# Kernel tuning notes

Measured on AMD Instinct MI355X. Metric: run time of the kernel, lower is better.

Reference implementation:

```python
import jax, jax.numpy as jnp
import numpy as np

N_EXPERTS = 8
TOP_K = 2
LB_COEF = 0.01
D_MODEL = 1024
D_FF = 4096


def setup_inputs() -> dict:
    key = jax.random.key(0)
    k_x, k_r, k_w1, k_w2, k_w3 = jax.random.split(key, 5)
    x = jax.random.normal(k_x, (2, 1024, D_MODEL), dtype=jnp.float32)
    # nn.Linear(d_model, n_experts, bias=False).weight has shape (E, d_model)
    router_w = jax.random.normal(k_r, (N_EXPERTS, D_MODEL), dtype=jnp.float32) * 0.02
    # stacked expert weights; stored pre-transposed for x @ W contractions
    w1 = jax.random.normal(k_w1, (N_EXPERTS, D_MODEL, D_FF), dtype=jnp.float32) * 0.02
    w3 = jax.random.normal(k_w3, (N_EXPERTS, D_MODEL, D_FF), dtype=jnp.float32) * 0.02
    w2 = jax.random.normal(k_w2, (N_EXPERTS, D_FF, D_MODEL), dtype=jnp.float32) * 0.02
    return {"x": x, "router_w": router_w, "w1": w1, "w3": w3, "w2": w2}


def reference(x, router_w, w1, w3, w2):
    B, T, C = x.shape
    xf = x.reshape(-1, C)                      # (N, C), N = B*T
    N = xf.shape[0]

    router_logits = xf @ router_w.T            # (N, E)
    top_v, top_i = jax.lax.top_k(router_logits, TOP_K)
    top_p = jax.nn.softmax(top_v, axis=-1)     # (N, K)

    # combine weight per (token, expert): sum of top-k probs routed to expert e
    comb = jnp.zeros((N, N_EXPERTS), dtype=xf.dtype)
    comb = comb.at[jnp.arange(N)[:, None], top_i].add(top_p)  # (N, E)

    # grouped SwiGLU FFN across all experts (dense-equivalent of masked loop;
    # tokens with zero combine weight contribute nothing)
    gate = jax.nn.silu(jnp.einsum("tc,ecf->etf", xf, w1))     # (E, N, F)
    up = jnp.einsum("tc,ecf->etf", xf, w3)                    # (E, N, F)
    expert_out = jnp.einsum("etf,efc->etc", gate * up, w2)    # (E, N, C)
    out = jnp.einsum("etc,te->tc", expert_out, comb)          # (N, C)

    router_probs = jax.nn.softmax(router_logits, axis=-1)
    expert_probs = router_probs.mean(axis=0)                  # (E,)
    aux_loss = LB_COEF * N_EXPERTS * jnp.sum(expert_probs * expert_probs)

    return out.reshape(B, T, C), aux_loss
```

## Files before the change

### kernel.cpp

```cpp
#include <hip/hip_runtime.h>
#include <hip/hip_bf16.h>
#include <hip/hip_fp16.h>

#define NTOK 2048
#define DM   1024
#define DF   4096
#define NE   8
#define NROWS (NTOK * 2)
#define NSPLIT 4
#define KSPL (DF / NSPLIT)
#define FFN1_NG (32 * 16 * 8)

typedef _Float16 f16x8 __attribute__((ext_vector_type(8)));
typedef float    f32x4 __attribute__((ext_vector_type(4)));
typedef unsigned u32x2 __attribute__((ext_vector_type(2)));

__device__ __forceinline__ void gload_lds16(const void* g, void* l) {
    __builtin_amdgcn_global_load_lds(
        (const __attribute__((address_space(1))) void*)g,
        (__attribute__((address_space(3))) void*)l, 16, 0, 0);
}

__device__ __forceinline__ u32x2 pack4(float4 v) {
    _Float16 a = (_Float16)v.x, b = (_Float16)v.y,
             c = (_Float16)v.z, d = (_Float16)v.w;
    unsigned ua = __builtin_bit_cast(unsigned short, a);
    unsigned ub = __builtin_bit_cast(unsigned short, b);
    unsigned uc = __builtin_bit_cast(unsigned short, c);
    unsigned ud = __builtin_bit_cast(unsigned short, d);
    u32x2 r;
    r[0] = ua | (ub << 16);
    r[1] = uc | (ud << 16);
    return r;
}

__global__ void k_init(int* counts, float* probs_sum) {
    int i = threadIdx.x;
    if (i < NE) { counts[i] = 0; probs_sum[i] = 0.f; }
}

__device__ __forceinline__ void transpose_tile(
    float* tile ,
    const float* __restrict__ src, _Float16* __restrict__ dst,
    int K, int N, int k0, int n0, int tid)
{
    int tk = tid >> 4, tn = (tid & 15) << 2;
#pragma unroll
    for (int r = 0; r < 4; r++) {
        float4 v = *(const float4*)(src + (size_t)(k0 + tk + (r << 4)) * N + n0 + tn);
        float* trow = &tile[(tk + (r << 4)) * 65 + tn];
        trow[0] = v.x; trow[1] = v.y; trow[2] = v.z; trow[3] = v.w;
    }
    __syncthreads();
    int on = tid >> 2, ok = (tid & 3) << 4;
    unsigned pk[8];
#pragma unroll
    for (int p2 = 0; p2 < 8; p2++) {
        _Float16 a = (_Float16)tile[(ok + 2 * p2) * 65 + on];
        _Float16 b = (_Float16)tile[(ok + 2 * p2 + 1) * 65 + on];
        pk[p2] = (unsigned)(*(unsigned short*)&a) | ((unsigned)(*(unsigned short*)&b) << 16);
    }
    _Float16* d = dst + (size_t)(n0 + on) * K + k0 + ok;
    *(uint4*)d       = make_uint4(pk[0], pk[1], pk[2], pk[3]);
    *(uint4*)(d + 8) = make_uint4(pk[4], pk[5], pk[6], pk[7]);
}

__global__ __launch_bounds__(256) void k_pre(
    const float* __restrict__ x, const float* __restrict__ rw,
    const float* __restrict__ w1, const float* __restrict__ w3,
    _Float16* __restrict__ WA, _Float16* __restrict__ WB,
    int* counts, float* probs_sum,
    int* pair_exp, int* pair_pos, float* topp)
{
    __shared__ float smem[64 * 65];
    int bid = blockIdx.x;
    int tid = threadIdx.x;

    if (bid >= 128) {
        int t = bid - 128;
        int z = t >> 10, xy = t & 1023;
        int e = z & 7;
        const float* src = ((z < 8) ? w1 : w3) + (size_t)e * DM * DF;
        _Float16* dst = ((z < 8) ? WA : WB) + (size_t)e * DF * DM;
        transpose_tile(smem, src, dst, DM, DF, (xy >> 6) << 6, (xy & 63) << 6, tid);
        return;
    }

    float* lprobs = smem;
    int* lcount = (int*)(smem + 8);
    int* lbase  = (int*)(smem + 16);
    if (tid < NE) { lprobs[tid] = 0.f; lcount[tid] = 0; }
    __syncthreads();

    int l16 = tid & 15;
    int t = bid * 16 + (tid >> 4);

    const float* xt = x + (size_t)t * DM;
    float acc[NE];
#pragma unroll
    for (int e = 0; e < NE; e++) acc[e] = 0.f;

#pragma unroll
    for (int i0 = 0; i0 < DM; i0 += 64) {
        int i = i0 + l16 * 4;
        float4 xv = *(const float4*)(xt + i);
#pragma unroll
        for (int e = 0; e < NE; e++) {
            float4 wv = *(const float4*)(rw + e * DM + i);
            acc[e] = fmaf(xv.x, wv.x, acc[e]);
            acc[e] = fmaf(xv.y, wv.y, acc[e]);
            acc[e] = fmaf(xv.z, wv.z, acc[e]);
            acc[e] = fmaf(xv.w, wv.w, acc[e]);
        }
    }
#pragma unroll
    for (int m = 1; m < 16; m <<= 1)
#pragma unroll
        for (int e = 0; e < NE; e++)
            acc[e] += __shfl_xor(acc[e], m);

    int i0e = 0, i1e = 0, r0 = 0, r1 = 0;
    if (l16 == 0) {
        float mx = acc[0];
#pragma unroll
        for (int e = 1; e < NE; e++) mx = fmaxf(mx, acc[e]);
        float p[NE]; float s = 0.f;
#pragma unroll
        for (int e = 0; e < NE; e++) { p[e] = expf(acc[e] - mx); s += p[e]; }
        float inv = 1.f / s;
#pragma unroll
        for (int e = 0; e < NE; e++) atomicAdd(&lprobs[e], p[e] * inv);

        i0e = 0;
#pragma unroll
        for (int e = 1; e < NE; e++) if (acc[e] > acc[i0e]) i0e = e;
        i1e = (i0e == 0) ? 1 : 0;
#pragma unroll
        for (int e = 0; e < NE; e++) if (e != i0e && acc[e] > acc[i1e]) i1e = e;

        float e1 = expf(acc[i1e] - acc[i0e]);
        float den = 1.f / (1.f + e1);
        topp[t * 2 + 0] = den;
        topp[t * 2 + 1] = e1 * den;
        pair_exp[t * 2 + 0] = i0e;
        pair_exp[t * 2 + 1] = i1e;
        r0 = atomicAdd(&lcount[i0e], 1);
        r1 = atomicAdd(&lcount[i1e], 1);
    }
    __syncthreads();
    if (tid < NE) {
        lbase[tid] = atomicAdd(&counts[tid], lcount[tid]);
        atomicAdd(&probs_sum[tid], lprobs[tid]);
    }
    __syncthreads();
    if (l16 == 0) {
        pair_pos[t * 2 + 0] = lbase[i0e] + r0;
        pair_pos[t * 2 + 1] = lbase[i1e] + r1;
    }
}

__global__ void k_offsets(const int* counts, const float* probs_sum,
                          int* eoff, float* out_aux)
{
    if (threadIdx.x == 0 && blockIdx.x == 0) {
        int off = 0;
        for (int e = 0; e < NE; e++) { eoff[e] = off; off += counts[e]; }
        eoff[NE] = off;
        float aux = 0.f;
        for (int e = 0; e < NE; e++) {
            float ep = probs_sum[e] / (float)NTOK;
            aux += ep * ep;
        }
        out_aux[0] = 0.01f * (float)NE * aux;
    }
}

__global__ __launch_bounds__(256) void k_gather(
    const float* __restrict__ x, const int* __restrict__ pair_exp,
    const int* __restrict__ pair_pos, const int* __restrict__ eoff,
    _Float16* __restrict__ Xg)
{
    int b = blockIdx.x;
    int t = b >> 1, s = b & 1;
    int e = pair_exp[t * 2 + s];
    int row = eoff[e] + pair_pos[t * 2 + s];
    int c = threadIdx.x << 2;
    float4 v = *(const float4*)(x + (size_t)t * DM + c);
    u32x2 o = pack4(v);
    *(u32x2*)(Xg + (size_t)row * DM + c) = o;
}

__global__ __launch_bounds__(256) void k_transpose(
    const float* __restrict__ W, _Float16* __restrict__ Wt, int K, int N)
{
    __shared__ float tile[64 * 65];
    int e = blockIdx.z;
    transpose_tile(tile, W + (size_t)e * K * N, Wt + (size_t)e * N * K,
                   K, N, blockIdx.y << 6, blockIdx.x << 6, threadIdx.x);
}

__global__ __launch_bounds__(256, 2) void k_ffn1(
    const _Float16* __restrict__ A, const _Float16* __restrict__ B1t,
    const _Float16* __restrict__ B3t, _Float16* __restrict__ H,
    const int* __restrict__ counts, const int* __restrict__ eoff,
    const float* __restrict__ w2, _Float16* __restrict__ W2T)
{
    __shared__ __align__(16) unsigned char smem[49152];
    int bid = blockIdx.x;
    int tid = threadIdx.x;

    if (bid >= FFN1_NG) {
        int t = bid - FFN1_NG;
        int e = t >> 10, xy = t & 1023;
        transpose_tile((float*)smem, w2 + (size_t)e * DF * DM,
                       W2T + (size_t)e * DM * DF,
                       DF, DM, (xy >> 4) << 6, (xy & 15) << 6, tid);
        return;
    }

    int e = bid >> 9;
    int m0 = ((bid >> 5) & 15) << 7;
    int n0 = (bid & 31) << 7;
    int cnt = counts[e];
    if (m0 >= cnt) return;
    int rb = eoff[e];

    int lane = tid & 63, w = tid >> 6;
    int wr = (w >> 1) << 6, wc = (w & 1) << 6;
    int l15 = lane & 15, l4 = lane >> 4;

    const _Float16* Ab  = A   + (size_t)(rb + m0) * DM;
    const _Float16* B1b = B1t + ((size_t)e * DF + n0) * DM;
    const _Float16* B3b = B3t + ((size_t)e * DF + n0) * DM;

    int c0 = tid, c1 = tid + 256;
    int r0c = c0 >> 2, s0c = (c0 & 3) ^ ((r0c >> 1) & 3);
    int r1c = c1 >> 2, s1c = (c1 & 3) ^ ((r1c >> 1) & 3);
    size_t g0 = (size_t)r0c * DM + (s0c << 3);
    size_t g1 = (size_t)r1c * DM + (s1c << 3);

    f32x4 accg[4][4], accu[4][4];
#pragma unroll
    for (int i = 0; i < 4; i++)
#pragma unroll
        for (int j = 0; j < 4; j++) {
            accg[i][j] = (f32x4){0.f, 0.f, 0.f, 0.f};
            accu[i][j] = (f32x4){0.f, 0.f, 0.f, 0.f};
        }

    auto STAGE = [&](unsigned char* buf, int k0) {
        gload_lds16(Ab  + g0 + k0, buf + (c0 << 4));
        gload_lds16(Ab  + g1 + k0, buf + (c1 << 4));
        gload_lds16(B1b + g0 + k0, buf + 8192 + (c0 << 4));
        gload_lds16(B1b + g1 + k0, buf + 8192 + (c1 << 4));
        gload_lds16(B3b + g0 + k0, buf + 16384 + (c0 << 4));
        gload_lds16(B3b + g1 + k0, buf + 16384 + (c1 << 4));
    };
    auto COMPUTE = [&](unsigned char* buf) {
        f16x8 af[4], b1f[4], b3f[4];
#pragma unroll
        for (int i = 0; i < 4; i++) {
            int r = wr + (i << 4) + l15;
            int s = l4 ^ ((r >> 1) & 3);
            af[i] = *(const f16x8*)(buf + (r << 6) + (s << 4));
        }
#pragma unroll
        for (int j = 0; j < 4; j++) {
            int r = wc + (j << 4) + l15;
            int s = l4 ^ ((r >> 1) & 3);
            int o = (r << 6) + (s << 4);
            b1f[j] = *(const f16x8*)(buf + 8192 + o);
            b3f[j] = *(const f16x8*)(buf + 16384 + o);
        }
#pragma unroll
        for (int i = 0; i < 4; i++)
#pragma unroll
            for (int j = 0; j < 4; j++) {
                accg[i][j] = __builtin_amdgcn_mfma_f32_16x16x32_f16(af[i], b1f[j], accg[i][j], 0, 0, 0);
                accu[i][j] = __builtin_amdgcn_mfma_f32_16x16x32_f16(af[i], b3f[j], accu[i][j], 0, 0, 0);
            }
    };

    unsigned char* bufA = smem;
    unsigned char* bufB = smem + 24576;
    STAGE(bufA, 0);
    __syncthreads();
    for (int k = 0; k < DM; k += 64) {
        STAGE(bufB, k + 32);
        COMPUTE(bufA);
        __syncthreads();
        if (k + 64 < DM) STAGE(bufA, k + 64);
        COMPUTE(bufB);
        __syncthreads();
    }

#pragma unroll
    for (int i = 0; i < 4; i++) {
#pragma unroll
        for (int rr = 0; rr < 4; rr++) {
            int m = m0 + wr + (i << 4) + (l4 << 2) + rr;
            if (m < cnt) {
                size_t go = (size_t)(rb + m) * DF + n0 + wc + l15;
#pragma unroll
                for (int j = 0; j < 4; j++) {
                    float g = accg[i][j][rr];
                    float u = accu[i][j][rr];
                    float h = g / (1.f + __expf(-g)) * u;
                    H[go + (size_t)(j << 4)] = (_Float16)h;
                }
            }
        }
    }
}

__global__ __launch_bounds__(256, 3) void k_gemm2(
    const _Float16* __restrict__ A, const _Float16* __restrict__ Bt,
    float* __restrict__ Yp,
    const int* __restrict__ counts, const int* __restrict__ eoff)
{
    __shared__ __align__(16) unsigned char smem[32768];
    int z = blockIdx.z;
    int e = z >> 2, sp = z & 3;
    int cnt = counts[e];
    int m0 = blockIdx.y << 7;
    if (m0 >= cnt) return;
    int n0 = blockIdx.x << 7;
    int rb = eoff[e];

    int tid = threadIdx.x;
    int lane = tid & 63, w = tid >> 6;
    int wr = (w >> 1) << 6, wc = (w & 1) << 6;
    int l15 = lane & 15, l4 = lane >> 4;

    const _Float16* Ab = A + (size_t)(rb + m0) * DF;
    const _Float16* Bb = Bt + ((size_t)e * DM + n0) * DF;

    int c0 = tid, c1 = tid + 256;
    int r0c = c0 >> 2, s0c = (c0 & 3) ^ ((r0c >> 1) & 3);
    int r1c = c1 >> 2, s1c = (c1 & 3) ^ ((r1c >> 1) & 3);
    size_t g0 = (size_t)r0c * DF + (s0c << 3);
    size_t g1 = (size_t)r1c * DF + (s1c << 3);

    f32x4 acc[4][4];
#pragma unroll
    for (int i = 0; i < 4; i++)
#pragma unroll
        for (int j = 0; j < 4; j++) acc[i][j] = (f32x4){0.f, 0.f, 0.f, 0.f};

    auto STAGE = [&](unsigned char* buf, int k0) {
        gload_lds16(Ab + g0 + k0, buf + (c0 << 4));
        gload_lds16(Ab + g1 + k0, buf + (c1 << 4));
        gload_lds16(Bb + g0 + k0, buf + 8192 + (c0 << 4));
        gload_lds16(Bb + g1 + k0, buf + 8192 + (c1 << 4));
    };
    auto COMPUTE = [&](unsigned char* buf) {
        f16x8 af[4], bfr[4];
#pragma unroll
        for (int i = 0; i < 4; i++) {
            int r = wr + (i << 4) + l15;
            int s = l4 ^ ((r >> 1) & 3);
            af[i] = *(const f16x8*)(buf + (r << 6) + (s << 4));
        }
#pragma unroll
        for (int j = 0; j < 4; j++) {
            int r = wc + (j << 4) + l15;
            int s = l4 ^ ((r >> 1) & 3);
            bfr[j] = *(const f16x8*)(buf + 8192 + (r << 6) + (s << 4));
        }
#pragma unroll
        for (int i = 0; i < 4; i++)
#pragma unroll
            for (int j = 0; j < 4; j++)
                acc[i][j] = __builtin_amdgcn_mfma_f32_16x16x32_f16(af[i], bfr[j], acc[i][j], 0, 0, 0);
    };

    unsigned char* bufA = smem;
    unsigned char* bufB = smem + 16384;
    int kbase = sp * KSPL;
    STAGE(bufA, kbase);
    __syncthreads();
    for (int k = 0; k < KSPL; k += 64) {
        STAGE(bufB, kbase + k + 32);
        COMPUTE(bufA);
        __syncthreads();
        if (k + 64 < KSPL) STAGE(bufA, kbase + k + 64);
        COMPUTE(bufB);
        __syncthreads();
    }

    float* Yo = Yp + (size_t)sp * NROWS * DM;
#pragma unroll
    for (int i = 0; i < 4; i++) {
#pragma unroll
        for (int rr = 0; rr < 4; rr++) {
            int m = m0 + wr + (i << 4) + (l4 << 2) + rr;
            if (m < cnt) {
                size_t go = (size_t)(rb + m) * DM + n0 + wc + l15;
#pragma unroll
                for (int j = 0; j < 4; j++)
                    Yo[go + (size_t)(j << 4)] = acc[i][j][rr];
            }
        }
    }
}

__global__ __launch_bounds__(256) void k_combine(
    const float* __restrict__ Yp,
    const int* __restrict__ pair_exp, const int* __restrict__ pair_pos,
    const float* __restrict__ topp, const int* __restrict__ eoff,
    float* __restrict__ out)
{
    int t = blockIdx.x;
    int c4 = threadIdx.x * 4;
    int e0 = pair_exp[t * 2], e1 = pair_exp[t * 2 + 1];
    size_t r0 = (size_t)(eoff[e0] + pair_pos[t * 2]);
    size_t r1 = (size_t)(eoff[e1] + pair_pos[t * 2 + 1]);
    float p0 = topp[t * 2], p1 = topp[t * 2 + 1];

    float4 a = make_float4(0.f, 0.f, 0.f, 0.f);
    float4 b = make_float4(0.f, 0.f, 0.f, 0.f);
#pragma unroll
    for (int sp = 0; sp < NSPLIT; sp++) {
        const float* base = Yp + (size_t)sp * NROWS * DM;
        float4 va = *(const float4*)&base[r0 * DM + c4];
        float4 vb = *(const float4*)&base[r1 * DM + c4];
        a.x += va.x; a.y += va.y; a.z += va.z; a.w += va.w;
        b.x += vb.x; b.y += vb.y; b.z += vb.z; b.w += vb.w;
    }
    float4 o;
    o.x = p0 * a.x + p1 * b.x;
    o.y = p0 * a.y + p1 * b.y;
    o.z = p0 * a.z + p1 * b.z;
    o.w = p0 * a.w + p1 * b.w;
    *(float4*)&out[(size_t)t * DM + c4] = o;
}

extern "C" void kernel_launch(void* const* d_in, const int* in_sizes, int n_in,
                              void* d_out, int out_size, void* d_ws, size_t ws_size,
                              hipStream_t stream)
{
    const float* x  = (const float*)d_in[0];
    const float* rw = (const float*)d_in[1];
    const float* w1 = (const float*)d_in[2];
    const float* w3 = (const float*)d_in[3];
    const float* w2 = (const float*)d_in[4];
    float* out = (float*)d_out;

    char* ws = (char*)d_ws;
    int*   counts    = (int*)ws;
    float* probs_sum = (float*)(ws + 64);
    int*   eoff      = (int*)(ws + 128);
    int*   pair_exp  = (int*)(ws + 256);
    int*   pair_pos  = (int*)(ws + 256 + NROWS * 4);
    float* topp      = (float*)(ws + 256 + 2 * NROWS * 4);

    _Float16* Xg  = (_Float16*)(ws + ((size_t)1 << 20));
    _Float16* H   = (_Float16*)(ws + ((size_t)9 << 20));
    _Float16* WA  = (_Float16*)(ws + ((size_t)41 << 20));
    _Float16* WB  = (_Float16*)(ws + ((size_t)105 << 20));
    float*    Yp  = (float*)WB;
    _Float16* W2T = (_Float16*)(ws + ((size_t)169 << 20));

    bool fused = ws_size >= ((size_t)234 << 20);

    k_init<<<1, 64, 0, stream>>>(counts, probs_sum);
    k_pre<<<128 + 16384, 256, 0, stream>>>(x, rw, w1, w3, WA, WB,
                                           counts, probs_sum, pair_exp, pair_pos, topp);
    k_offsets<<<1, 1, 0, stream>>>(counts, probs_sum, eoff, out + (size_t)NTOK * DM);
    k_gather<<<NROWS, 256, 0, stream>>>(x, pair_exp, pair_pos, eoff, Xg);

    if (fused) {
        k_ffn1<<<FFN1_NG + 8192, 256, 0, stream>>>(Xg, WA, WB, H, counts, eoff, w2, W2T);
        k_gemm2<<<dim3(DM / 128, 16, NE * NSPLIT), 256, 0, stream>>>(H, W2T, Yp, counts, eoff);
    } else {
        k_ffn1<<<FFN1_NG, 256, 0, stream>>>(Xg, WA, WB, H, counts, eoff, w2, nullptr);
        k_transpose<<<dim3(DM / 64, DF / 64, NE), 256, 0, stream>>>(w2, WA, DF, DM);
        k_gemm2<<<dim3(DM / 128, 16, NE * NSPLIT), 256, 0, stream>>>(H, WA, Yp, counts, eoff);
    }

    k_combine<<<NTOK, 256, 0, stream>>>(Yp, pair_exp, pair_pos, topp, eoff, out);
}
```

Baseline: 296.3 us.

## Use partial vmcnt waits and MFMA priority in FFN GEMM pipelines

Both expert GEMM kernels now issue the next LDS stage and then wait only until the current stage's global-to-LDS loads have landed (partial s_waitcnt vmcnt), instead of a full __syncthreads that drains every outstanding load. Sched barriers pin the instruction order, and s_setprio raises wave priority around the MFMA block. The goal is to keep the next tile's loads in flight while the current tile is computed. The risk is correctness if the vmcnt counts do not match the per-thread load count, and it relies on compiler scheduling staying fixed.

```diff
diff --git a/kernel.cpp b/kernel.cpp
--- a/kernel.cpp
+++ b/kernel.cpp
@@ -256,7 +256,7 @@
         gload_lds16(B3b + g0 + k0, buf + 16384 + (c0 << 4));
         gload_lds16(B3b + g1 + k0, buf + 16384 + (c1 << 4));
     };
-    auto COMPUTE = [&](unsigned char* buf) {
+    auto COMPUTE = [&](const unsigned char* buf) {
         f16x8 af[4], b1f[4], b3f[4];
 #pragma unroll
         for (int i = 0; i < 4; i++) {
@@ -272,6 +272,7 @@
             b1f[j] = *(const f16x8*)(buf + 8192 + o);
             b3f[j] = *(const f16x8*)(buf + 16384 + o);
         }
+        __builtin_amdgcn_s_setprio(1);
 #pragma unroll
         for (int i = 0; i < 4; i++)
 #pragma unroll
@@ -279,20 +280,28 @@
                 accg[i][j] = __builtin_amdgcn_mfma_f32_16x16x32_f16(af[i], b1f[j], accg[i][j], 0, 0, 0);
                 accu[i][j] = __builtin_amdgcn_mfma_f32_16x16x32_f16(af[i], b3f[j], accu[i][j], 0, 0, 0);
             }
+        __builtin_amdgcn_s_setprio(0);
     };
 
-    unsigned char* bufA = smem;
-    unsigned char* bufB = smem + 24576;
-    STAGE(bufA, 0);
-    __syncthreads();
-    for (int k = 0; k < DM; k += 64) {
-        STAGE(bufB, k + 32);
-        COMPUTE(bufA);
-        __syncthreads();
-        if (k + 64 < DM) STAGE(bufA, k + 64);
-        COMPUTE(bufB);
-        __syncthreads();
-    }
+    unsigned char* cur = smem;
+    unsigned char* nxt = smem + 24576;
+
+    STAGE(cur, 0);
+    for (int k = 32; k < DM; k += 32) {
+        STAGE(nxt, k);
+        __builtin_amdgcn_sched_barrier(0);
+        asm volatile("s_waitcnt vmcnt(6)" ::: "memory");
+        __builtin_amdgcn_s_barrier();
+        __builtin_amdgcn_sched_barrier(0);
+        COMPUTE(cur);
+        __builtin_amdgcn_sched_barrier(0);
+        __builtin_amdgcn_s_barrier();
+        unsigned char* tp = cur; cur = nxt; nxt = tp;
+    }
+    asm volatile("s_waitcnt vmcnt(0)" ::: "memory");
+    __builtin_amdgcn_s_barrier();
+    __builtin_amdgcn_sched_barrier(0);
+    COMPUTE(cur);
 
 #pragma unroll
     for (int i = 0; i < 4; i++) {
@@ -353,7 +362,7 @@
         gload_lds16(Bb + g0 + k0, buf + 8192 + (c0 << 4));
         gload_lds16(Bb + g1 + k0, buf + 8192 + (c1 << 4));
     };
-    auto COMPUTE = [&](unsigned char* buf) {
+    auto COMPUTE = [&](const unsigned char* buf) {
         f16x8 af[4], bfr[4];
 #pragma unroll
         for (int i = 0; i < 4; i++) {
@@ -367,26 +376,35 @@
             int s = l4 ^ ((r >> 1) & 3);
             bfr[j] = *(const f16x8*)(buf + 8192 + (r << 6) + (s << 4));
         }
+        __builtin_amdgcn_s_setprio(1);
 #pragma unroll
         for (int i = 0; i < 4; i++)
 #pragma unroll
             for (int j = 0; j < 4; j++)
                 acc[i][j] = __builtin_amdgcn_mfma_f32_16x16x32_f16(af[i], bfr[j], acc[i][j], 0, 0, 0);
+        __builtin_amdgcn_s_setprio(0);
     };
 
-    unsigned char* bufA = smem;
-    unsigned char* bufB = smem + 16384;
+    unsigned char* cur = smem;
+    unsigned char* nxt = smem + 16384;
     int kbase = sp * KSPL;
-    STAGE(bufA, kbase);
-    __syncthreads();
-    for (int k = 0; k < KSPL; k += 64) {
-        STAGE(bufB, kbase + k + 32);
-        COMPUTE(bufA);
-        __syncthreads();
-        if (k + 64 < KSPL) STAGE(bufA, kbase + k + 64);
-        COMPUTE(bufB);
-        __syncthreads();
-    }
+
+    STAGE(cur, kbase);
+    for (int k = 32; k < KSPL; k += 32) {
+        STAGE(nxt, kbase + k);
+        __builtin_amdgcn_sched_barrier(0);
+        asm volatile("s_waitcnt vmcnt(4)" ::: "memory");
+        __builtin_amdgcn_s_barrier();
+        __builtin_amdgcn_sched_barrier(0);
+        COMPUTE(cur);
+        __builtin_amdgcn_sched_barrier(0);
+        __builtin_amdgcn_s_barrier();
+        unsigned char* tp = cur; cur = nxt; nxt = tp;
+    }
+    asm volatile("s_waitcnt vmcnt(0)" ::: "memory");
+    __builtin_amdgcn_s_barrier();
+    __builtin_amdgcn_sched_barrier(0);
+    COMPUTE(cur);
 
     float* Yo = Yp + (size_t)sp * NROWS * DM;
 #pragma unroll
```

Measured after the change: 292.6 us (median of 2 runs). Within noise of the previous version (-1.3%).
